# Kernel tuning notes

Measured on AMD Instinct MI355X. Metric: run time of the kernel, lower is better.

Reference implementation:

```python
import jax, jax.numpy as jnp
import numpy as np

DIM = 768
NUM_EXPERTS = 64
N_FRQ = 2048
TOPK = 2
B = 32
ALPHA = 300.0


def setup_inputs() -> dict:
    key = jax.random.key(0)
    k1, k2, k3, k4 = jax.random.split(key, 4)
    cls_token = jax.random.normal(k1, (B, DIM), dtype=jnp.float32)
    W_router = jax.random.normal(k2, (NUM_EXPERTS, DIM), dtype=jnp.float32) * 0.02
    b_router = jnp.zeros((NUM_EXPERTS,), dtype=jnp.float32)
    coeff = jax.random.normal(k3, (NUM_EXPERTS, N_FRQ), dtype=jnp.float32)
    # distinct flat indices into the dim*dim grid (mirrors torch.randperm slices)
    perm = jax.random.permutation(k4, DIM * DIM)
    list_indices = perm[: NUM_EXPERTS * N_FRQ].reshape(NUM_EXPERTS, N_FRQ).astype(jnp.int32)
    return {
        "cls_token": cls_token,
        "W_router": W_router,
        "b_router": b_router,
        "coeff": coeff,
        "list_indices": list_indices,
    }


def reference(cls_token, W_router, b_router, coeff, list_indices):
    # router + topk expert selection
    logits = cls_token @ W_router.T + b_router                  # [B, E]
    probs = jax.nn.softmax(logits, axis=-1)
    w, idx = jax.lax.top_k(probs, TOPK)                          # [B, topk]
    w = w / jnp.sum(w, axis=-1, keepdims=True)

    # gather per-expert frequency indices and coefficients
    sel_idx = list_indices[idx]                                  # [B, topk, n_frq]
    vals = coeff[idx] * w[..., None]                             # [B, topk, n_frq]

    # scatter-add into flat frequency grid
    b_ix = jnp.arange(B)[:, None, None]                          # [B,1,1]
    mask = jnp.zeros((B, DIM * DIM), dtype=cls_token.dtype)
    mask = mask.at[b_ix, sel_idx].add(vals)
    mask = mask.reshape(B, DIM, DIM)

    # dense inverse FFT2 over the (mostly-zero) grid
    out = jnp.fft.ifft2(mask, axes=(-2, -1)).real * ALPHA        # [B, dim, dim]
    return out
```

## Files before the change

kernel.cpp:

```cpp
#include <hip/hip_runtime.h>
#include <hip/hip_bf16.h>

#define DIM 768
#define NE 64
#define NFRQ 2048
#define NB 32
#define HALF 384
#define KROW 1536
#define KG 768
#define TWO_PI 6.283185307179586f
#define INV768 (1.0f / 768.0f)
#define SCALE (300.0f / (float)(DIM * DIM))

typedef __attribute__((ext_vector_type(8))) short bf16x8;
typedef __attribute__((ext_vector_type(4))) float f32x4;

__global__ __launch_bounds__(256) void prep_kernel(const float* __restrict__ cls,
                                                   const float* __restrict__ W,
                                                   const float* __restrict__ bias,
                                                   const float* __restrict__ coeff,
                                                   const int* __restrict__ lidx,
                                                   int* __restrict__ row_start,
                                                   float2* __restrict__ s_cv,
                                                   __hip_bfloat16* __restrict__ A,
                                                   float2* __restrict__ T2) {
  int bid = blockIdx.x;
  int tid = threadIdx.x;

  if (bid >= 32 + 2 * 192) {
    int c = bid - (32 + 2 * 192);
    for (int x = tid; x < HALF; x += 256) {
      float prod = (float)(c * x);
      float f, sn, cs;
      float rev = prod * INV768;
      asm("v_fract_f32 %0, %1" : "=v"(f) : "v"(rev));
      asm("v_sin_f32 %0, %1" : "=v"(sn) : "v"(f));
      asm("v_cos_f32 %0, %1" : "=v"(cs) : "v"(f));
      T2[(size_t)c * HALF + x] = make_float2(cs, -sn);
    }
    return;
  }
  if (bid >= 32) {
    int idx = bid - 32;
    int y = 2 * (idx % 192) + (idx / 192);
    if (tid < 96) {
      int r0 = tid * 4;
      union { __hip_bfloat16 h[4]; ushort4 v; } uc, us;
#pragma unroll
      for (int j = 0; j < 4; ++j) {
        int m = (y * (r0 + j)) % DIM;
        float s, c;
        sincosf((TWO_PI / (float)DIM) * (float)m, &s, &c);
        uc.h[j] = __float2bfloat16(c);
        us.h[j] = __float2bfloat16(s);
      }
      *(ushort4*)(A + (size_t)idx * KG + r0)        = uc.v;
      *(ushort4*)(A + (size_t)idx * KG + HALF + r0) = us.v;
    }
    return;
  }

  int b = bid;
  __shared__ int cnt[DIM];
  __shared__ int base[DIM];
  __shared__ int wsum[4];
  __shared__ int sel_i[2];
  __shared__ float sel_f[2];
  float* part   = (float*)cnt;
  float* logits = (float*)base;

  {
    int e = tid & 63, q = tid >> 6;
    const float* c = cls + b * DIM + q * 192;
    const float* w = W + e * DIM + q * 192;
    float acc = 0.f;
#pragma unroll 4
    for (int i = 0; i < 192; i += 4) {
      float4 cv4 = *(const float4*)(c + i);
      float4 wv4 = *(const float4*)(w + i);
      acc += cv4.x * wv4.x + cv4.y * wv4.y + cv4.z * wv4.z + cv4.w * wv4.w;
    }
    part[q * 64 + e] = acc;
    __syncthreads();
    if (tid < NE)
      logits[tid] = part[tid] + part[64 + tid] + part[128 + tid] + part[192 + tid] + bias[tid];
    __syncthreads();
    if (tid == 0) {
      int i0 = 0; float l0 = logits[0];
      for (int i = 1; i < NE; ++i) { float v = logits[i]; if (v > l0) { l0 = v; i0 = i; } }
      int i1 = -1; float l1 = -3.4e38f;
      for (int i = 0; i < NE; ++i) {
        if (i == i0) continue;
        float v = logits[i]; if (v > l1) { l1 = v; i1 = i; }
      }
      float w0 = 1.f / (1.f + expf(l1 - l0));
      sel_i[0] = i0; sel_i[1] = i1;
      sel_f[0] = w0; sel_f[1] = 1.f - w0;
    }
    __syncthreads();
  }
  int e0 = sel_i[0], e1 = sel_i[1];
  float w0 = sel_f[0], w1 = sel_f[1];

  for (int i = tid; i < DIM; i += 256) cnt[i] = 0;
  __syncthreads();
  for (int k = tid; k < 2 * NFRQ; k += 256) {
    int t = k >> 11, j = k & (NFRQ - 1);
    int e = t ? e1 : e0;
    int f = lidx[e * NFRQ + j];
    atomicAdd(&cnt[f / DIM], 1);
  }
  __syncthreads();
  {
    int s0 = cnt[3 * tid], s1 = cnt[3 * tid + 1], s2 = cnt[3 * tid + 2];
    int sum = s0 + s1 + s2;
    int lane = tid & 63, wid = tid >> 6;
    int v = sum;
#pragma unroll
    for (int d = 1; d < 64; d <<= 1) {
      int u = __shfl_up(v, d);
      if (lane >= d) v += u;
    }
    if (lane == 63) wsum[wid] = v;
    __syncthreads();
    int woff = 0;
#pragma unroll
    for (int w = 0; w < 4; ++w) if (w < wid) woff += wsum[w];
    int excl = woff + v - sum;
    int* rsg = row_start + b * (DIM + 1);
    base[3 * tid]     = excl;
    base[3 * tid + 1] = excl + s0;
    base[3 * tid + 2] = excl + s0 + s1;
    rsg[3 * tid]     = excl;
    rsg[3 * tid + 1] = excl + s0;
    rsg[3 * tid + 2] = excl + s0 + s1;
    if (tid == 255) rsg[DIM] = excl + sum;
  }
  __syncthreads();
  for (int i = tid; i < DIM; i += 256) cnt[i] = 0;
  __syncthreads();
  for (int k = tid; k < 2 * NFRQ; k += 256) {
    int t = k >> 11, j = k & (NFRQ - 1);
    int e = t ? e1 : e0;
    float w = t ? w1 : w0;
    int f = lidx[e * NFRQ + j];
    int r = f / DIM, c = f - r * DIM;
    int pos = base[r] + atomicAdd(&cnt[r], 1);
    s_cv[b * 4096 + pos] = make_float2(__uint_as_float((unsigned)c * 3072u),
                                       coeff[e * NFRQ + j] * w * SCALE);
  }
}

__global__ __launch_bounds__(256) void stage1_kernel(const int* __restrict__ row_start,
                                                     const float2* __restrict__ s_cv,
                                                     const float2* __restrict__ T2,
                                                     __hip_bfloat16* __restrict__ BT) {
  int b = blockIdx.y;
  int rg = blockIdx.x;
  int tid = threadIdx.x;
  int lane = tid & 63, w = tid >> 6;
  __shared__ __hip_bfloat16 lreP[8][HALF];
  __shared__ __hip_bfloat16 limP[8][HALF];
  __shared__ __hip_bfloat16 lreM[8][HALF];
  __shared__ __hip_bfloat16 limM[8][HALF];
  const int* rs = row_start + b * (DIM + 1);
  const float2* cv = s_cv + b * 4096;
  __hip_bfloat16* BTb = BT + (size_t)b * HALF * KROW;
  int rowBase = rg * 8;

#pragma unroll
  for (int rr = 0; rr < 2; ++rr) {
    int rslot = 2 * w + rr;
    int rp = rowBase + rslot;
    int sA = rs[rp],       eA = rs[rp + 1];
    int sB = rs[rp + 384], eB = rs[rp + 385];
    float accA[12], accB[12];
#pragma unroll
    for (int k = 0; k < 12; ++k) { accA[k] = 0.f; accB[k] = 0.f; }

    int pa = sA, pb = sB;
    for (; pa < eA && pb < eB; ++pa, ++pb) {
      float2 a  = cv[pa];
      float2 bq = cv[pb];
      const char* ta = (const char*)T2 + (size_t)__float_as_uint(a.x);
      const char* tb = (const char*)T2 + (size_t)__float_as_uint(bq.x);
      float va = a.y, vb = bq.y;
#pragma unroll
      for (int j = 0; j < 3; ++j) {
        float4 t0 = *(const float4*)(ta + lane * 16 + j * 1024);
        float4 t1 = *(const float4*)(tb + lane * 16 + j * 1024);
        accA[4 * j + 0] += va * t0.x; accB[4 * j + 0] += vb * t1.x;
        accA[4 * j + 1] += va * t0.y; accB[4 * j + 1] += vb * t1.y;
        accA[4 * j + 2] += va * t0.z; accB[4 * j + 2] += vb * t1.z;
        accA[4 * j + 3] += va * t0.w; accB[4 * j + 3] += vb * t1.w;
      }
    }
    for (; pa < eA; ++pa) {
      float2 a = cv[pa];
      const char* ta = (const char*)T2 + (size_t)__float_as_uint(a.x);
      float va = a.y;
#pragma unroll
      for (int j = 0; j < 3; ++j) {
        float4 t0 = *(const float4*)(ta + lane * 16 + j * 1024);
        accA[4 * j + 0] += va * t0.x;
        accA[4 * j + 1] += va * t0.y;
        accA[4 * j + 2] += va * t0.z;
        accA[4 * j + 3] += va * t0.w;
      }
    }
    for (; pb < eB; ++pb) {
      float2 bq = cv[pb];
      const char* tb = (const char*)T2 + (size_t)__float_as_uint(bq.x);
      float vb = bq.y;
#pragma unroll
      for (int j = 0; j < 3; ++j) {
        float4 t1 = *(const float4*)(tb + lane * 16 + j * 1024);
        accB[4 * j + 0] += vb * t1.x;
        accB[4 * j + 1] += vb * t1.y;
        accB[4 * j + 2] += vb * t1.z;
        accB[4 * j + 3] += vb * t1.w;
      }
    }
#pragma unroll
    for (int j = 0; j < 3; ++j) {
      union { __hip_bfloat16 h[2]; unsigned u; } rP, iP, rM, iM;
      rP.h[0] = __float2bfloat16(accA[4 * j + 0] + accB[4 * j + 0]);
      rP.h[1] = __float2bfloat16(accA[4 * j + 2] + accB[4 * j + 2]);
      iP.h[0] = __float2bfloat16(accA[4 * j + 1] + accB[4 * j + 1]);
      iP.h[1] = __float2bfloat16(accA[4 * j + 3] + accB[4 * j + 3]);
      rM.h[0] = __float2bfloat16(accA[4 * j + 0] - accB[4 * j + 0]);
      rM.h[1] = __float2bfloat16(accA[4 * j + 2] - accB[4 * j + 2]);
      iM.h[0] = __float2bfloat16(accA[4 * j + 1] - accB[4 * j + 1]);
      iM.h[1] = __float2bfloat16(accA[4 * j + 3] - accB[4 * j + 3]);
      int x = 2 * lane + 128 * j;
      *(unsigned*)&lreP[rslot][x] = rP.u;
      *(unsigned*)&limP[rslot][x] = iP.u;
      *(unsigned*)&lreM[rslot][x] = rM.u;
      *(unsigned*)&limM[rslot][x] = iM.u;
    }
  }
  __syncthreads();
  for (int x = tid; x < HALF; x += 256) {
    union { ushort h[8]; uint4 v; } uP, vP, uM, vM;
#pragma unroll
    for (int k = 0; k < 8; ++k) {
      uP.h[k] = *(const ushort*)&lreP[k][x];
      vP.h[k] = *(const ushort*)&limP[k][x];
      uM.h[k] = *(const ushort*)&lreM[k][x];
      vM.h[k] = *(const ushort*)&limM[k][x];
    }
    __hip_bfloat16* dst = BTb + (size_t)x * KROW + rowBase;
    *(uint4*)(dst)        = uP.v;
    *(uint4*)(dst + 384)  = vP.v;
    *(uint4*)(dst + 768)  = uM.v;
    *(uint4*)(dst + 1152) = vM.v;
  }
}

__device__ inline void gload_lds16(const void* g, void* l) {
  __builtin_amdgcn_global_load_lds((const __attribute__((address_space(1))) void*)g,
                                   (__attribute__((address_space(3))) void*)l, 16, 0, 0);
}

__global__ __launch_bounds__(256) void gemm_kernel(const __hip_bfloat16* __restrict__ A,
                                                   const __hip_bfloat16* __restrict__ BT,
                                                   const int* __restrict__ row_start,
                                                   const float2* __restrict__ s_cv,
                                                   float* __restrict__ C) {
  int bid = blockIdx.x;
  int tid = threadIdx.x;
  __shared__ __align__(16) __hip_bfloat16 As[2][64 * 64];
  __shared__ __align__(16) __hip_bfloat16 Bs[2][64 * 64];

  if (bid < 4 * NB) {
    int slice = bid & 3, b = bid >> 2;
    float* ob = C + (size_t)b * DIM * DIM;
    if (slice == 3) {
      for (int x = tid; x < HALF; x += 256) {
        const __hip_bfloat16* btx = BT + ((size_t)(b * HALF + x)) * KROW;
        float acc = 0.f;
        for (int r = 0; r < HALF; r += 8) {
          union { uint4 v4; __hip_bfloat16 h[8]; } u;
          u.v4 = *(const uint4*)(btx + r);
#pragma unroll
          for (int q = 0; q < 8; ++q) {
            float v = __bfloat162float(u.h[q]);
            acc += (q & 1) ? -v : v;
          }
        }
        int xm = x ? DIM - x : 0;
        ob[(size_t)HALF * DIM + x]  = acc;
        ob[(size_t)HALF * DIM + xm] = acc;
      }
      return;
    }
    float* Re384 = (float*)As;
    const int* rs = row_start + b * (DIM + 1);
    const float2* cv = s_cv + b * 4096;
    for (int r = tid; r < DIM; r += 256) {
      int s = rs[r], e = rs[r + 1];
      float acc = 0.f;
      for (int p = s; p < e; ++p) {
        float2 c = cv[p];
        int ci = (int)(__float_as_uint(c.x) / 3072u);
        acc += (ci & 1) ? -c.y : c.y;
      }
      Re384[r] = acc;
    }
    __syncthreads();
    int y = slice * 129 + tid;
    if (tid < 129 && y <= HALF) {
      float yf = (float)y;
      float a0 = 0.f, a1 = 0.f, a2 = 0.f, a3 = 0.f;
      for (int r = 0; r < DIM; r += 4) {
        float f0, f1, f2, f3, c0, c1, c2, c3;
        float v0 = (yf * (float)(r + 0)) * INV768;
        float v1 = (yf * (float)(r + 1)) * INV768;
        float v2 = (yf * (float)(r + 2)) * INV768;
        float v3 = (yf * (float)(r + 3)) * INV768;
        asm("v_fract_f32 %0, %1" : "=v"(f0) : "v"(v0));
        asm("v_fract_f32 %0, %1" : "=v"(f1) : "v"(v1));
        asm("v_fract_f32 %0, %1" : "=v"(f2) : "v"(v2));
        asm("v_fract_f32 %0, %1" : "=v"(f3) : "v"(v3));
        asm("v_cos_f32 %0, %1" : "=v"(c0) : "v"(f0));
        asm("v_cos_f32 %0, %1" : "=v"(c1) : "v"(f1));
        asm("v_cos_f32 %0, %1" : "=v"(c2) : "v"(f2));
        asm("v_cos_f32 %0, %1" : "=v"(c3) : "v"(f3));
        a0 += Re384[r + 0] * c0;
        a1 += Re384[r + 1] * c1;
        a2 += Re384[r + 2] * c2;
        a3 += Re384[r + 3] * c3;
      }
      float acc = (a0 + a1) + (a2 + a3);
      int ym = y ? DIM - y : 0;
      ob[(size_t)y  * DIM + HALF] = acc;
      ob[(size_t)ym * DIM + HALF] = acc;
    }
    return;
  }

  int gbid = bid - 4 * NB;
  int swz = (gbid & 7) * 144 + (gbid >> 3);
  int b = swz / 36; int rem = swz - b * 36;
  int par = rem / 18; int r2 = rem - par * 18;
  int bx = r2 / 3, by = r2 % 3;

  float* Cp = C + (size_t)b * DIM * DIM;
  int y0 = by * 64, x0 = bx * 64;

  int wv = tid >> 6, lane = tid & 63;
  int wr = wv >> 1, wc = wv & 1;
  int lhi = lane >> 4, llo = lane & 15;

  int c0 = tid, c1 = tid + 256;
  int row0 = c0 >> 3, row1 = c1 >> 3;
  int so0 = (((c0 & 7) ^ (row0 & 7))) * 8;
  int so1 = (((c1 & 7) ^ (row1 & 7))) * 8;

  f32x4 acc1[2][2] = {};
  f32x4 acc2[2][2] = {};

  const __hip_bfloat16* A0 = A  + ((size_t)(par * 192 + y0 + row0)) * KG + so0;
  const __hip_bfloat16* A1 = A  + ((size_t)(par * 192 + y0 + row1)) * KG + so1;
  const __hip_bfloat16* B0 = BT + ((size_t)(b * HALF + x0 + row0)) * KROW + par * KG + so0;
  const __hip_bfloat16* B1 = BT + ((size_t)(b * HALF + x0 + row1)) * KROW + par * KG + so1;

  gload_lds16(A0, As[0] + c0 * 8);
  gload_lds16(A1, As[0] + c1 * 8);
  gload_lds16(B0, Bs[0] + c0 * 8);
  gload_lds16(B1, Bs[0] + c1 * 8);
  __syncthreads();

  auto step = [&](int t, f32x4 (&acc)[2][2], bool last) {
    int cur = t & 1;
    if (!last) {
      int ktn = (t + 1) * 64;
      gload_lds16(A0 + ktn, As[cur ^ 1] + c0 * 8);
      gload_lds16(A1 + ktn, As[cur ^ 1] + c1 * 8);
      gload_lds16(B0 + ktn, Bs[cur ^ 1] + c0 * 8);
      gload_lds16(B1 + ktn, Bs[cur ^ 1] + c1 * 8);
    }
    bf16x8 af[2][2], bfr[2][2];
#pragma unroll
    for (int i = 0; i < 2; ++i)
#pragma unroll
      for (int kh = 0; kh < 2; ++kh) {
        int row = wr * 32 + i * 16 + llo;
        int phys = ((lhi + 4 * kh) ^ (llo & 7)) * 8;
        af[i][kh] = *(const bf16x8*)(As[cur] + row * 64 + phys);
      }
#pragma unroll
    for (int j = 0; j < 2; ++j)
#pragma unroll
      for (int kh = 0; kh < 2; ++kh) {
        int row = wc * 32 + j * 16 + llo;
        int phys = ((lhi + 4 * kh) ^ (llo & 7)) * 8;
        bfr[j][kh] = *(const bf16x8*)(Bs[cur] + row * 64 + phys);
      }
#pragma unroll
    for (int kh = 0; kh < 2; ++kh)
#pragma unroll
      for (int i = 0; i < 2; ++i)
#pragma unroll
        for (int j = 0; j < 2; ++j)
          acc[i][j] = __builtin_amdgcn_mfma_f32_16x16x32_bf16(af[i][kh], bfr[j][kh],
                                                              acc[i][j], 0, 0, 0);
    if (!last) __syncthreads();
  };

  for (int t = 0; t < 6; ++t)  step(t, acc1, false);
  for (int t = 6; t < 12; ++t) step(t, acc2, t == 11);

#pragma unroll
  for (int i = 0; i < 2; ++i) {
#pragma unroll
    for (int j = 0; j < 2; ++j) {
      int x = x0 + wc * 32 + j * 16 + llo;
      int xm = x ? DIM - x : 0;
#pragma unroll
      for (int q = 0; q < 4; ++q) {
        int tt = y0 + wr * 32 + i * 16 + lhi * 4 + q;
        int y = 2 * tt + par;
        int ym = y ? DIM - y : 0;
        float c1 = acc1[i][j][q], c2 = acc2[i][j][q];
        float vd = c1 + c2;
        float vs = c1 - c2;
        Cp[(size_t)y  * DIM + x]  = vd;
        Cp[(size_t)ym * DIM + xm] = vd;
        Cp[(size_t)y  * DIM + xm] = vs;
        Cp[(size_t)ym * DIM + x]  = vs;
      }
    }
  }
}

extern "C" void kernel_launch(void* const* d_in, const int* in_sizes, int n_in,
                              void* d_out, int out_size, void* d_ws, size_t ws_size,
                              hipStream_t stream) {
  const float* cls   = (const float*)d_in[0];
  const float* Wr    = (const float*)d_in[1];
  const float* br    = (const float*)d_in[2];
  const float* coeff = (const float*)d_in[3];
  const int*   lidx  = (const int*)d_in[4];
  float* out = (float*)d_out;

  char* ws = (char*)d_ws;
  int*    row_start = (int*)(ws + 0);
  float2* s_cv      = (float2*)(ws + 98944);
  __hip_bfloat16* A  = (__hip_bfloat16*)(ws + 1147520);
  float2* T2        = (float2*)(ws + 1737344);
  __hip_bfloat16* BT = (__hip_bfloat16*)(ws + 4096640);

  prep_kernel<<<32 + 384 + DIM, 256, 0, stream>>>(cls, Wr, br, coeff, lidx,
                                                  row_start, s_cv, A, T2);
  stage1_kernel<<<dim3(48, NB), 256, 0, stream>>>(row_start, s_cv, T2, BT);
  gemm_kernel<<<4 * NB + 1152, 256, 0, stream>>>(A, BT, row_start, s_cv, out);
}
```

Measured before the change: 113.2 us.

## Retile stage1 over column chunks with 32 rows per block and merged row loop

```diff
diff --git a/kernel.cpp b/kernel.cpp
--- a/kernel.cpp
+++ b/kernel.cpp
@@ -155,105 +155,77 @@
                                                      const float2* __restrict__ s_cv,
                                                      const float2* __restrict__ T2,
                                                      __hip_bfloat16* __restrict__ BT) {
-  int b = blockIdx.y;
+  int b = blockIdx.z;
+  int xg = blockIdx.y;
   int rg = blockIdx.x;
   int tid = threadIdx.x;
   int lane = tid & 63, w = tid >> 6;
-  __shared__ __hip_bfloat16 lreP[8][HALF];
-  __shared__ __hip_bfloat16 limP[8][HALF];
-  __shared__ __hip_bfloat16 lreM[8][HALF];
-  __shared__ __hip_bfloat16 limM[8][HALF];
+  __shared__ __hip_bfloat16 lds[4][32][132];
   const int* rs = row_start + b * (DIM + 1);
   const float2* cv = s_cv + b * 4096;
-  __hip_bfloat16* BTb = BT + (size_t)b * HALF * KROW;
-  int rowBase = rg * 8;
-
-#pragma unroll
-  for (int rr = 0; rr < 2; ++rr) {
-    int rslot = 2 * w + rr;
-    int rp = rowBase + rslot;
-    int sA = rs[rp],       eA = rs[rp + 1];
-    int sB = rs[rp + 384], eB = rs[rp + 385];
-    float accA[12], accB[12];
-#pragma unroll
-    for (int k = 0; k < 12; ++k) { accA[k] = 0.f; accB[k] = 0.f; }
-
-    int pa = sA, pb = sB;
-    for (; pa < eA && pb < eB; ++pa, ++pb) {
-      float2 a  = cv[pa];
-      float2 bq = cv[pb];
-      const char* ta = (const char*)T2 + (size_t)__float_as_uint(a.x);
-      const char* tb = (const char*)T2 + (size_t)__float_as_uint(bq.x);
-      float va = a.y, vb = bq.y;
-#pragma unroll
-      for (int j = 0; j < 3; ++j) {
-        float4 t0 = *(const float4*)(ta + lane * 16 + j * 1024);
-        float4 t1 = *(const float4*)(tb + lane * 16 + j * 1024);
-        accA[4 * j + 0] += va * t0.x; accB[4 * j + 0] += vb * t1.x;
-        accA[4 * j + 1] += va * t0.y; accB[4 * j + 1] += vb * t1.y;
-        accA[4 * j + 2] += va * t0.z; accB[4 * j + 2] += vb * t1.z;
-        accA[4 * j + 3] += va * t0.w; accB[4 * j + 3] += vb * t1.w;
-      }
-    }
-    for (; pa < eA; ++pa) {
-      float2 a = cv[pa];
-      const char* ta = (const char*)T2 + (size_t)__float_as_uint(a.x);
-      float va = a.y;
-#pragma unroll
-      for (int j = 0; j < 3; ++j) {
-        float4 t0 = *(const float4*)(ta + lane * 16 + j * 1024);
-        accA[4 * j + 0] += va * t0.x;
-        accA[4 * j + 1] += va * t0.y;
-        accA[4 * j + 2] += va * t0.z;
-        accA[4 * j + 3] += va * t0.w;
-      }
-    }
-    for (; pb < eB; ++pb) {
-      float2 bq = cv[pb];
-      const char* tb = (const char*)T2 + (size_t)__float_as_uint(bq.x);
-      float vb = bq.y;
-#pragma unroll
-      for (int j = 0; j < 3; ++j) {
-        float4 t1 = *(const float4*)(tb + lane * 16 + j * 1024);
-        accB[4 * j + 0] += vb * t1.x;
-        accB[4 * j + 1] += vb * t1.y;
-        accB[4 * j + 2] += vb * t1.z;
-        accB[4 * j + 3] += vb * t1.w;
-      }
-    }
-#pragma unroll
-    for (int j = 0; j < 3; ++j) {
-      union { __hip_bfloat16 h[2]; unsigned u; } rP, iP, rM, iM;
-      rP.h[0] = __float2bfloat16(accA[4 * j + 0] + accB[4 * j + 0]);
-      rP.h[1] = __float2bfloat16(accA[4 * j + 2] + accB[4 * j + 2]);
-      iP.h[0] = __float2bfloat16(accA[4 * j + 1] + accB[4 * j + 1]);
-      iP.h[1] = __float2bfloat16(accA[4 * j + 3] + accB[4 * j + 3]);
-      rM.h[0] = __float2bfloat16(accA[4 * j + 0] - accB[4 * j + 0]);
-      rM.h[1] = __float2bfloat16(accA[4 * j + 2] - accB[4 * j + 2]);
-      iM.h[0] = __float2bfloat16(accA[4 * j + 1] - accB[4 * j + 1]);
-      iM.h[1] = __float2bfloat16(accA[4 * j + 3] - accB[4 * j + 3]);
-      int x = 2 * lane + 128 * j;
-      *(unsigned*)&lreP[rslot][x] = rP.u;
-      *(unsigned*)&limP[rslot][x] = iP.u;
-      *(unsigned*)&lreM[rslot][x] = rM.u;
-      *(unsigned*)&limM[rslot][x] = iM.u;
-    }
-  }
-  __syncthreads();
-  for (int x = tid; x < HALF; x += 256) {
-    union { ushort h[8]; uint4 v; } uP, vP, uM, vM;
-#pragma unroll
-    for (int k = 0; k < 8; ++k) {
-      uP.h[k] = *(const ushort*)&lreP[k][x];
-      vP.h[k] = *(const ushort*)&limP[k][x];
-      uM.h[k] = *(const ushort*)&lreM[k][x];
-      vM.h[k] = *(const ushort*)&limM[k][x];
-    }
-    __hip_bfloat16* dst = BTb + (size_t)x * KROW + rowBase;
-    *(uint4*)(dst)        = uP.v;
-    *(uint4*)(dst + 384)  = vP.v;
-    *(uint4*)(dst + 768)  = uM.v;
-    *(uint4*)(dst + 1152) = vM.v;
+  int rowBase = rg * 32;
+  size_t xbyte = (size_t)xg * 1024 + (size_t)lane * 16;
+
+  for (int rr = 0; rr < 4; ++rr) {
+    int slot0 = w * 8 + 2 * rr;
+    int p0 = rowBase + slot0;
+    int sA0 = rs[p0],       nA0 = rs[p0 + 1]   - sA0;
+    int sB0 = rs[p0 + 384], nB0 = rs[p0 + 385] - sB0;
+    int sA1 = rs[p0 + 1],   nA1 = rs[p0 + 2]   - sA1;
+    int sB1 = rs[p0 + 385], nB1 = rs[p0 + 386] - sB1;
+    int kmax = nA0 > nB0 ? nA0 : nB0;
+    int km2  = nA1 > nB1 ? nA1 : nB1;
+    if (km2 > kmax) kmax = km2;
+    float a0[4] = {0,0,0,0}, b0[4] = {0,0,0,0};
+    float a1[4] = {0,0,0,0}, b1[4] = {0,0,0,0};
+    for (int k = 0; k < kmax; ++k) {
+      if (k < nA0) {
+        float2 c = cv[sA0 + k];
+        float4 t = *(const float4*)((const char*)T2 + (size_t)__float_as_uint(c.x) + xbyte);
+        a0[0] += c.y * t.x; a0[1] += c.y * t.y; a0[2] += c.y * t.z; a0[3] += c.y * t.w;
+      }
+      if (k < nB0) {
+        float2 c = cv[sB0 + k];
+        float4 t = *(const float4*)((const char*)T2 + (size_t)__float_as_uint(c.x) + xbyte);
+        b0[0] += c.y * t.x; b0[1] += c.y * t.y; b0[2] += c.y * t.z; b0[3] += c.y * t.w;
+      }
+      if (k < nA1) {
+        float2 c = cv[sA1 + k];
+        float4 t = *(const float4*)((const char*)T2 + (size_t)__float_as_uint(c.x) + xbyte);
+        a1[0] += c.y * t.x; a1[1] += c.y * t.y; a1[2] += c.y * t.z; a1[3] += c.y * t.w;
+      }
+      if (k < nB1) {
+        float2 c = cv[sB1 + k];
+        float4 t = *(const float4*)((const char*)T2 + (size_t)__float_as_uint(c.x) + xbyte);
+        b1[0] += c.y * t.x; b1[1] += c.y * t.y; b1[2] += c.y * t.z; b1[3] += c.y * t.w;
+      }
+    }
+    int xl = 2 * lane;
+    union { __hip_bfloat16 h[2]; unsigned u; } u0;
+#pragma unroll
+    for (int s = 0; s < 2; ++s) {
+      const float* aa = s ? a1 : a0;
+      const float* bb = s ? b1 : b0;
+      int slot = slot0 + s;
+      u0.h[0] = __float2bfloat16(aa[0] + bb[0]); u0.h[1] = __float2bfloat16(aa[2] + bb[2]);
+      *(unsigned*)&lds[0][slot][xl] = u0.u;
+      u0.h[0] = __float2bfloat16(aa[1] + bb[1]); u0.h[1] = __float2bfloat16(aa[3] + bb[3]);
+      *(unsigned*)&lds[1][slot][xl] = u0.u;
+      u0.h[0] = __float2bfloat16(aa[0] - bb[0]); u0.h[1] = __float2bfloat16(aa[2] - bb[2]);
+      *(unsigned*)&lds[2][slot][xl] = u0.u;
+      u0.h[0] = __float2bfloat16(aa[1] - bb[1]); u0.h[1] = __float2bfloat16(aa[3] - bb[3]);
+      *(unsigned*)&lds[3][slot][xl] = u0.u;
+    }
+  }
+  __syncthreads();
+  for (int i = tid; i < 512; i += 256) {
+    int a = i >> 7, x = i & 127;
+    union { ushort h[32]; uint4 v[4]; } u;
+#pragma unroll
+    for (int k = 0; k < 32; ++k) u.h[k] = *(const ushort*)&lds[a][k][x];
+    __hip_bfloat16* dst = BT + ((size_t)(b * HALF + xg * 128 + x)) * KROW + a * HALF + rowBase;
+#pragma unroll
+    for (int q = 0; q < 4; ++q) *(uint4*)(dst + q * 8) = u.v[q];
   }
 }
 
@@ -453,6 +425,6 @@
 
   prep_kernel<<<32 + 384 + DIM, 256, 0, stream>>>(cls, Wr, br, coeff, lidx,
                                                   row_start, s_cv, A, T2);
-  stage1_kernel<<<dim3(48, NB), 256, 0, stream>>>(row_start, s_cv, T2, BT);
+  stage1_kernel<<<dim3(12, 3, NB), 256, 0, stream>>>(row_start, s_cv, T2, BT);
   gemm_kernel<<<4 * NB + 1152, 256, 0, stream>>>(A, BT, row_start, s_cv, out);
 }
```

After: 146.7 us. 1.3x slower.
